# Kernel optimization log

Hardware: AMD Instinct MI355X
Metric: run time of the kernel (lower is better)

## Reference

```python
import jax, jax.numpy as jnp
import numpy as np

B, S, D = 2, 2048, 1024
H, KVH, HD = 16, 4, 64
ROPE_THETA = 10000.0


def rotate_half(x):
    h = x.shape[-1] // 2
    return jnp.concatenate([-x[..., h:], x[..., :h]], axis=-1)


def setup_inputs() -> dict:
    key = jax.random.key(0)
    k = jax.random.split(key, 6)
    x = jax.random.normal(k[0], (B, S, D), dtype=jnp.float32)
    # real RoPE tables: [S, HD//2]
    inv_freq = 1.0 / (ROPE_THETA ** (jnp.arange(0, HD, 2, dtype=jnp.float32) / HD))
    t = jnp.arange(S, dtype=jnp.float32)
    freqs = jnp.outer(t, inv_freq)  # [S, HD/2]
    cos = jnp.cos(freqs)
    sin = jnp.sin(freqs)
    # causal additive mask [1,1,S,S]
    neg = jnp.float32(-1e9)
    mask = jnp.where(jnp.tril(jnp.ones((S, S), dtype=bool)), 0.0, neg)[None, None]
    scale = 0.02
    wq = jax.random.normal(k[1], (D, H * HD), dtype=jnp.float32) * scale
    wk = jax.random.normal(k[2], (D, KVH * HD), dtype=jnp.float32) * scale
    wv = jax.random.normal(k[3], (D, KVH * HD), dtype=jnp.float32) * scale
    wo = jax.random.normal(k[4], (H * HD, D), dtype=jnp.float32) * scale
    return {"x": x, "cos": cos, "sin": sin, "mask": mask,
            "wq": wq, "wk": wk, "wv": wv, "wo": wo}


def reference(x, cos, sin, mask, wq, wk, wv, wo):
    b, s, d = x.shape
    hd = 2 * cos.shape[-1]
    h = wq.shape[1] // hd
    kvh = wk.shape[1] // hd
    n_rep = h // kvh

    q = (x @ wq).reshape(b, s, h, hd)
    k = (x @ wk).reshape(b, s, kvh, hd)
    v = (x @ wv).reshape(b, s, kvh, hd)

    # RoPE: cos/sin [S, hd/2] -> [1, s, 1, hd] via self-concat (rotate_half style)
    c = jnp.concatenate([cos[:s], cos[:s]], axis=-1)[None, :, None, :]
    sn = jnp.concatenate([sin[:s], sin[:s]], axis=-1)[None, :, None, :]
    q = q * c + rotate_half(q) * sn
    k = k * c + rotate_half(k) * sn

    new_k, new_v = k, v  # kv cache (pre-repeat)

    # GQA: repeat each kv head n_rep times contiguously (== expand+reshape)
    if n_rep > 1:
        k = jnp.repeat(k, n_rep, axis=2)
        v = jnp.repeat(v, n_rep, axis=2)

    scores = jnp.einsum('bqhd,bkhd->bhqk', q, k) / jnp.sqrt(jnp.float32(hd))
    scores = scores + mask
    attn = jax.nn.softmax(scores.astype(jnp.float32), axis=-1).astype(q.dtype)
    out = jnp.einsum('bhqk,bkhd->bqhd', attn, v).reshape(b, s, h * hd)
    out = out @ wo
    return (out, new_k, new_v)
```

## Files before the change

kernel.cpp:

```cpp
#include <hip/hip_runtime.h>
#include <hip/hip_bf16.h>

constexpr int B_ = 2, S_ = 2048, D_ = 1024, H_ = 16, KVH_ = 4, HD_ = 64;

typedef __attribute__((ext_vector_type(8))) short short8;
typedef __attribute__((ext_vector_type(4))) float f32x4;
typedef __attribute__((ext_vector_type(16))) float f32x16;

__device__ inline short f2b(float x) {
  unsigned u = __float_as_uint(x);
  return (short)((u + 0x7fffu + ((u >> 16) & 1u)) >> 16);
}
__device__ inline unsigned pkbf2(float lo, float hi) {
  __hip_bfloat162 h = __float22bfloat162_rn(float2{lo, hi});
  return *(unsigned*)&h;
}

__device__ inline void async16(void* lds, const void* g) {
  __builtin_amdgcn_global_load_lds(
      (const __attribute__((address_space(1))) unsigned int*)g,
      (__attribute__((address_space(3))) unsigned int*)lds, 16, 0, 0);
}

__global__ __launch_bounds__(256) void prep_kernel(
    const float* __restrict__ x, short* __restrict__ xb,
    const float* __restrict__ wq, const float* __restrict__ wk,
    const float* __restrict__ wv, const float* __restrict__ wo,
    short* __restrict__ wt, short* __restrict__ wot) {
  __shared__ short ts[64][66];
  const int tid = threadIdx.x;
  if (blockIdx.x < 4096) {
    const int idx = (blockIdx.x * 256 + tid) * 4;
    float4 v = *(const float4*)(x + idx);
    short4 o;
    o.x = f2b(v.x); o.y = f2b(v.y); o.z = f2b(v.z); o.w = f2b(v.w);
    *(short4*)(xb + idx) = o;
    return;
  }
  const int bid = blockIdx.x - 4096;
  const int z = bid >> 8, bi = (bid >> 4) & 15, bj = bid & 15;
  const float* W;
  short* dst;
  int N;
  if (z == 0)      { W = wq; dst = wt;                       N = 1024; }
  else if (z == 1) { W = wo; dst = wot;                      N = 1024; }
  else if (z == 2) { W = wk; dst = wt + (size_t)1024 * 1024; N = 256; }
  else             { W = wv; dst = wt + (size_t)1280 * 1024; N = 256; }
  if (bj * 64 >= N) return;
#pragma unroll
  for (int i = 0; i < 16; ++i) {
    int idx = tid + i * 256;
    int r = idx >> 6, c = idx & 63;
    ts[r][c] = f2b(W[(size_t)(bi * 64 + r) * N + bj * 64 + c]);
  }
  __syncthreads();
#pragma unroll
  for (int i = 0; i < 16; ++i) {
    int idx = tid + i * 256;
    int cc = idx >> 6, rr = idx & 63;
    dst[(size_t)(bj * 64 + cc) * 1024 + bi * 64 + rr] = ts[rr][cc];
  }
}

struct GemmLdsDb {
  short As[2][128][32];
  short Bs[2][128][32];
};

__device__ inline void gemm_core_db(GemmLdsDb& lds, const short* __restrict__ A,
                                    const short* __restrict__ Bt, int K,
                                    int row0, int col0, int tid,
                                    f32x4 (&acc)[4][4]) {
  const int w = tid >> 6, lane = tid & 63;
  const int grp = lane >> 4, li = lane & 15;
  const int wr = w & 1, wc = w >> 1;
  const int lr = lane >> 2, ls = (lane & 3) * 8;
#pragma unroll
  for (int mt = 0; mt < 4; ++mt)
#pragma unroll
    for (int nt = 0; nt < 4; ++nt) acc[mt][nt] = (f32x4){0.f, 0.f, 0.f, 0.f};

  auto issue = [&](int bi, int k0) {
#pragma unroll
    for (int i = 0; i < 2; ++i) {
      const int r = i * 64 + w * 16;
      async16(&lds.As[bi][r][0], A + (size_t)(row0 + r + lr) * K + k0 + ls);
      async16(&lds.Bs[bi][r][0], Bt + (size_t)(col0 + r + lr) * K + k0 + ls);
    }
  };

  issue(0, 0);
  const int nk = K >> 5;
  for (int kk = 0; kk < nk; ++kk) {
    const int cur = kk & 1;
    __syncthreads();
    if (kk + 1 < nk) issue(cur ^ 1, (kk + 1) << 5);

    short8 af[4], bf[4];
#pragma unroll
    for (int mt = 0; mt < 4; ++mt)
      af[mt] = *(const short8*)&lds.As[cur][wr * 64 + mt * 16 + li][grp * 8];
#pragma unroll
    for (int nt = 0; nt < 4; ++nt)
      bf[nt] = *(const short8*)&lds.Bs[cur][wc * 64 + nt * 16 + li][grp * 8];
#pragma unroll
    for (int mt = 0; mt < 4; ++mt)
#pragma unroll
      for (int nt = 0; nt < 4; ++nt)
        acc[mt][nt] = __builtin_amdgcn_mfma_f32_16x16x32_bf16(
            af[mt], bf[nt], acc[mt][nt], 0, 0, 0);
  }
}

#define QSCALE 0.1803368801111f

__global__ __launch_bounds__(256) void gemm_qkv(
    const short* __restrict__ A, const short* __restrict__ Bt,
    const float* __restrict__ cs, const float* __restrict__ sn,
    short* __restrict__ qb, float* __restrict__ koutp, short* __restrict__ kb,
    float* __restrict__ voutp, short* __restrict__ vbT) {
  __shared__ GemmLdsDb lds;
  const int tid = threadIdx.x;
  const int w = tid >> 6, lane = tid & 63;
  const int grp = lane >> 4, li = lane & 15;
  const int wr = w & 1, wc = w >> 1;
  const int row0 = blockIdx.y * 128, col0 = blockIdx.x * 128;
  f32x4 acc[4][4];
  gemm_core_db(lds, A, Bt, D_, row0, col0, tid, acc);

  if (col0 < 1024) {
#pragma unroll
    for (int mt = 0; mt < 4; ++mt)
#pragma unroll
      for (int r = 0; r < 4; ++r) {
        const int row = row0 + wr * 64 + mt * 16 + grp * 4 + r;
        const int spos = row & (S_ - 1);
#pragma unroll
        for (int nt = 0; nt < 2; ++nt) {
          const int col = col0 + wc * 64 + nt * 16 + li;
          const int d = col & 63;
          const float c = cs[spos * 32 + d];
          const float s = sn[spos * 32 + d];
          const float x0 = acc[mt][nt][r], x1 = acc[mt][nt + 2][r];
          qb[(size_t)row * 1024 + col] = f2b((x0 * c - x1 * s) * QSCALE);
          qb[(size_t)row * 1024 + col + 32] = f2b((x1 * c + x0 * s) * QSCALE);
        }
      }
  } else if (col0 < 1280) {
#pragma unroll
    for (int mt = 0; mt < 4; ++mt)
#pragma unroll
      for (int r = 0; r < 4; ++r) {
        const int row = row0 + wr * 64 + mt * 16 + grp * 4 + r;
        const int spos = row & (S_ - 1);
#pragma unroll
        for (int nt = 0; nt < 2; ++nt) {
          const int kcol = col0 + wc * 64 + nt * 16 + li - 1024;
          const int d = kcol & 63;
          const float c = cs[spos * 32 + d];
          const float s = sn[spos * 32 + d];
          const float x0 = acc[mt][nt][r], x1 = acc[mt][nt + 2][r];
          const float k0v = x0 * c - x1 * s;
          const float k1v = x1 * c + x0 * s;
          koutp[(size_t)row * 256 + kcol] = k0v;
          koutp[(size_t)row * 256 + kcol + 32] = k1v;
          kb[(size_t)row * 256 + kcol] = f2b(k0v);
          kb[(size_t)row * 256 + kcol + 32] = f2b(k1v);
        }
      }
  } else {
#pragma unroll
    for (int mt = 0; mt < 4; ++mt)
#pragma unroll
      for (int nt = 0; nt < 4; ++nt) {
        const int vcol = col0 + wc * 64 + nt * 16 + li - 1280;
        const int row_base = row0 + wr * 64 + mt * 16 + grp * 4;
        short4 pk;
        float vv[4];
#pragma unroll
        for (int r = 0; r < 4; ++r) vv[r] = acc[mt][nt][r];
        pk.x = f2b(vv[0]); pk.y = f2b(vv[1]);
        pk.z = f2b(vv[2]); pk.w = f2b(vv[3]);
#pragma unroll
        for (int r = 0; r < 4; ++r)
          voutp[(size_t)(row_base + r) * 256 + vcol] = vv[r];
        const int b = row_base >> 11, s0 = row_base & (S_ - 1);
        *(short4*)&vbT[((size_t)(b * 256 + vcol)) * S_ + s0] = pk;
      }
  }
}

__global__ __launch_bounds__(128) void fattn_kernel(
    const short* __restrict__ qb, const short* __restrict__ kb,
    const short* __restrict__ vbT, short* __restrict__ o) {
  __shared__ float scr[64 * 33 + 32];

  const int tid = threadIdx.x;
  const int par = tid >> 6, lane = tid & 63;
  const int n32 = lane & 31, kg = lane >> 5;

  const int qt = 63 - (blockIdx.x >> 5);
  const int bh = blockIdx.x & 31;
  const int b = bh >> 4, h = bh & 15, kh = h >> 2;
  const int qq = qt >> 1, st = qt & 1;
  const int nt = qq + 1;

  const short* qp =
      qb + ((size_t)(b * S_ + qt * 32 + n32)) * 1024 + h * 64 + kg * 8;
  short8 qa[4];
#pragma unroll
  for (int ks = 0; ks < 4; ++ks) qa[ks] = *(const short8*)(qp + ks * 16);

  const short* kl = kb + ((size_t)(b * S_) + n32) * 256 + kh * 64 + kg * 8;
  const short* vl0 = vbT + ((size_t)(b * 256 + kh * 64 + n32)) * S_ + kg * 8;
  const short* vl1 = vl0 + (size_t)32 * S_;

  f32x16 zero16;
#pragma unroll
  for (int i = 0; i < 16; ++i) zero16[i] = 0.f;
  f32x16 Oa0 = zero16, Oa1 = zero16;
  float lreg = 0.f;

  auto loadK = [&](int t, short8 (&kr)[8]) {
    const short* kt = kl + (size_t)t * (64 * 256);
#pragma unroll
    for (int i = 0; i < 4; ++i) {
      kr[i] = *(const short8*)(kt + i * 16);
      kr[i + 4] = *(const short8*)(kt + 32 * 256 + i * 16);
    }
  };

  auto body = [&](int t, const short8 (&kr)[8]) {
    const bool diag = (t == qq);
    const short* vt0 = vl0 + t * 64;
    const short* vt1 = vl1 + t * 64;
    short8 vr[8];
#pragma unroll
    for (int kc = 0; kc < 4; ++kc) {
      vr[kc] = *(const short8*)(vt0 + kc * 16);
      vr[kc + 4] = *(const short8*)(vt1 + kc * 16);
    }
    unsigned pk[4][4];
#pragma unroll
    for (int s = 0; s < 2; ++s) {
      if (s == 1 && diag && st == 0) continue;
      f32x16 sv = __builtin_amdgcn_mfma_f32_32x32x16_bf16(kr[s * 4 + 0], qa[0],
                                                          zero16, 0, 0, 0);
      sv = __builtin_amdgcn_mfma_f32_32x32x16_bf16(kr[s * 4 + 1], qa[1], sv, 0,
                                                   0, 0);
      sv = __builtin_amdgcn_mfma_f32_32x32x16_bf16(kr[s * 4 + 2], qa[2], sv, 0,
                                                   0, 0);
      sv = __builtin_amdgcn_mfma_f32_32x32x16_bf16(kr[s * 4 + 3], qa[3], sv, 0,
                                                   0, 0);
      const bool dm = diag && (s == st);
      float e[16];
#pragma unroll
      for (int rr = 0; rr < 16; ++rr) {
        float v = __builtin_amdgcn_exp2f(sv[rr]);
        if (dm) {
          const int key32 = (rr & 3) + 8 * (rr >> 2) + 4 * kg;
          if (key32 > n32) v = 0.f;
        }
        e[rr] = v;
      }
      pk[2 * s][0] = pkbf2(e[0], e[1]);
      pk[2 * s][1] = pkbf2(e[2], e[3]);
      pk[2 * s][2] = pkbf2(e[4], e[5]);
      pk[2 * s][3] = pkbf2(e[6], e[7]);
      pk[2 * s + 1][0] = pkbf2(e[8], e[9]);
      pk[2 * s + 1][1] = pkbf2(e[10], e[11]);
      pk[2 * s + 1][2] = pkbf2(e[12], e[13]);
      pk[2 * s + 1][3] = pkbf2(e[14], e[15]);
      lreg += (((e[0] + e[1]) + (e[2] + e[3])) +
               ((e[4] + e[5]) + (e[6] + e[7]))) +
              (((e[8] + e[9]) + (e[10] + e[11])) +
               ((e[12] + e[13]) + (e[14] + e[15])));
    }

    auto pv = [&](int kc) {
      auto r02 =
          __builtin_amdgcn_permlane32_swap(pk[kc][0], pk[kc][2], false, false);
      auto r13 =
          __builtin_amdgcn_permlane32_swap(pk[kc][1], pk[kc][3], false, false);
      union { unsigned u[4]; short8 s8; } f;
      f.u[0] = r02[0]; f.u[1] = r13[0]; f.u[2] = r02[1]; f.u[3] = r13[1];
      Oa0 = __builtin_amdgcn_mfma_f32_32x32x16_bf16(vr[kc], f.s8, Oa0, 0, 0, 0);
      Oa1 = __builtin_amdgcn_mfma_f32_32x32x16_bf16(vr[kc + 4], f.s8, Oa1, 0,
                                                    0, 0);
    };
    if (diag && st == 0) {
      pv(0); pv(1);
    } else {
      pv(0); pv(1); pv(2); pv(3);
    }
  };

  {
    short8 kA[8], kB[8];
    int t = par;
    if (t < nt) {
      loadK(t, kA);
      while (true) {
        {
          const int tp = (t + 2 < nt) ? t + 2 : t;
          loadK(tp, kB);
          body(t, kA);
          t += 2;
          if (t >= nt) break;
        }
        {
          const int tp = (t + 2 < nt) ? t + 2 : t;
          loadK(tp, kA);
          body(t, kB);
          t += 2;
          if (t >= nt) break;
        }
      }
    }
  }

  lreg += __shfl_xor(lreg, 32);

  float* lb = scr + 64 * 33;
  if (par == 1) {
#pragma unroll
    for (int rr = 0; rr < 16; ++rr) {
      const int d0 = (rr & 3) + 8 * (rr >> 2) + 4 * kg;
      scr[d0 * 33 + n32] = Oa0[rr];
      scr[(d0 + 32) * 33 + n32] = Oa1[rr];
    }
    if (kg == 0) lb[n32] = lreg;
  }
  __syncthreads();
  if (par == 0) {
    const float inv = __builtin_amdgcn_rcpf(lreg + lb[n32]);
#pragma unroll
    for (int rr = 0; rr < 16; ++rr) {
      const int d0 = (rr & 3) + 8 * (rr >> 2) + 4 * kg;
      scr[d0 * 33 + n32] = (Oa0[rr] + scr[d0 * 33 + n32]) * inv;
      scr[(d0 + 32) * 33 + n32] = (Oa1[rr] + scr[(d0 + 32) * 33 + n32]) * inv;
    }
  }
  __syncthreads();
  {
    const int q = tid >> 2, seg = (tid & 3) * 16;
    const size_t gb = ((size_t)(b * S_ + qt * 32 + q)) * 1024 + h * 64 + seg;
    short8 t0, t1;
#pragma unroll
    for (int k2 = 0; k2 < 8; ++k2) {
      t0[k2] = f2b(scr[(seg + k2) * 33 + q]);
      t1[k2] = f2b(scr[(seg + 8 + k2) * 33 + q]);
    }
    *(short8*)(o + gb) = t0;
    *(short8*)(o + gb + 8) = t1;
  }
}

__global__ __launch_bounds__(256) void gemm_bt_f32(
    const short* __restrict__ A, const short* __restrict__ Bt,
    float* __restrict__ C, int N, int K) {
  __shared__ GemmLdsDb lds;
  const int tid = threadIdx.x;
  const int w = tid >> 6, lane = tid & 63;
  const int grp = lane >> 4, li = lane & 15;
  const int wr = w & 1, wc = w >> 1;
  const int row0 = blockIdx.y * 128, col0 = blockIdx.x * 128;
  f32x4 acc[4][4];
  gemm_core_db(lds, A, Bt, K, row0, col0, tid, acc);
#pragma unroll
  for (int mt = 0; mt < 4; ++mt)
#pragma unroll
    for (int nt = 0; nt < 4; ++nt)
#pragma unroll
      for (int r = 0; r < 4; ++r)
        C[(size_t)(row0 + wr * 64 + mt * 16 + grp * 4 + r) * N + col0 +
          wc * 64 + nt * 16 + li] = acc[mt][nt][r];
}

extern "C" void kernel_launch(void* const* d_in, const int* in_sizes, int n_in,
                              void* d_out, int out_size, void* d_ws,
                              size_t ws_size, hipStream_t stream) {
  const float* x  = (const float*)d_in[0];
  const float* cs = (const float*)d_in[1];
  const float* sn = (const float*)d_in[2];
  const float* wq = (const float*)d_in[4];
  const float* wk = (const float*)d_in[5];
  const float* wv = (const float*)d_in[6];
  const float* wo = (const float*)d_in[7];

  float* outp  = (float*)d_out;
  float* koutp = outp + (size_t)B_ * S_ * H_ * HD_;
  float* voutp = koutp + (size_t)B_ * S_ * KVH_ * HD_;

  char* p = (char*)d_ws;
  short* xb   = (short*)p; p += (size_t)B_ * S_ * D_ * 2;
  short* qb   = (short*)p; p += (size_t)B_ * S_ * H_ * HD_ * 2;
  short* kb   = (short*)p; p += (size_t)B_ * S_ * KVH_ * HD_ * 2;
  short* vbT  = (short*)p; p += (size_t)B_ * S_ * KVH_ * HD_ * 2;
  short* abuf = (short*)p; p += (size_t)B_ * S_ * H_ * HD_ * 2;
  short* wt   = (short*)p; p += (size_t)1536 * D_ * 2;
  short* wot  = (short*)p; p += (size_t)D_ * H_ * HD_ * 2;

  const int M = B_ * S_;

  prep_kernel<<<4096 + 1024, 256, 0, stream>>>(x, xb, wq, wk, wv, wo, wt,
                                               wot);

  gemm_qkv<<<dim3(1536 / 128, M / 128), 256, 0, stream>>>(
      xb, wt, cs, sn, qb, koutp, kb, voutp, vbT);

  fattn_kernel<<<64 * 32, 128, 0, stream>>>(qb, kb, vbT, abuf);

  gemm_bt_f32<<<dim3(1024 / 128, M / 128), 256, 0, stream>>>(abuf, wot, outp,
                                                             1024, 1024);
}
```

Before: 211.2 us.

## Store K and V in MFMA fragment-contiguous tiled layout for coalesced attention loads

The projection kernel now writes bf16 K and transposed V into a per-(batch,kv-head) tiled layout where each lane's 16-byte MFMA operand sits contiguously, so the attention kernel loads fragments with lane-linear, fully coalesced addresses instead of strided row accesses. The K prefetch for tile t+2 is moved inside the body after the V loads and made conditional, removing the redundant reload of the current tile at the end of the loop. The cost is scattered 2-byte stores in the prep kernel's epilogue, which may hurt write coalescing there.

```diff
diff --git a/kernel.cpp b/kernel.cpp
--- a/kernel.cpp
+++ b/kernel.cpp
@@ -152,11 +152,12 @@
 #pragma unroll
       for (int r = 0; r < 4; ++r) {
         const int row = row0 + wr * 64 + mt * 16 + grp * 4 + r;
-        const int spos = row & (S_ - 1);
+        const int bq = row >> 11, spos = row & (S_ - 1);
+        const int sb = spos >> 5, k32 = spos & 31;
 #pragma unroll
         for (int nt = 0; nt < 2; ++nt) {
           const int kcol = col0 + wc * 64 + nt * 16 + li - 1024;
-          const int d = kcol & 63;
+          const int khk = kcol >> 6, d = kcol & 63;
           const float c = cs[spos * 32 + d];
           const float s = sn[spos * 32 + d];
           const float x0 = acc[mt][nt][r], x1 = acc[mt][nt + 2][r];
@@ -164,8 +165,11 @@
           const float k1v = x1 * c + x0 * s;
           koutp[(size_t)row * 256 + kcol] = k0v;
           koutp[(size_t)row * 256 + kcol + 32] = k1v;
-          kb[(size_t)row * 256 + kcol] = f2b(k0v);
-          kb[(size_t)row * 256 + kcol + 32] = f2b(k1v);
+          short* kbase =
+              kb + (((size_t)(bq * 4 + khk) * 64 + sb) * 2048) + k32 * 8;
+          const int d2 = d + 32;
+          kbase[((d >> 4) * 2 + ((d >> 3) & 1)) * 256 + (d & 7)] = f2b(k0v);
+          kbase[((d2 >> 4) * 2 + ((d2 >> 3) & 1)) * 256 + (d2 & 7)] = f2b(k1v);
         }
       }
   } else {
@@ -184,8 +188,13 @@
 #pragma unroll
         for (int r = 0; r < 4; ++r)
           voutp[(size_t)(row_base + r) * 256 + vcol] = vv[r];
-        const int b = row_base >> 11, s0 = row_base & (S_ - 1);
-        *(short4*)&vbT[((size_t)(b * 256 + vcol)) * S_ + s0] = pk;
+        const int bq = row_base >> 11, s0 = row_base & (S_ - 1);
+        const int t = s0 >> 6, k64 = s0 & 63;
+        const int kc = k64 >> 4, kg8 = (k64 >> 3) & 1, k8 = k64 & 7;
+        const int khv = vcol >> 6, d = vcol & 63;
+        short* vb = vbT + (((size_t)(bq * 4 + khv) * 32 + t) * 4096) +
+                    (d >> 5) * 2048 + kc * 512 + kg8 * 256 + (d & 31) * 8 + k8;
+        *(short4*)vb = pk;
       }
   }
 }
@@ -211,9 +220,8 @@
 #pragma unroll
   for (int ks = 0; ks < 4; ++ks) qa[ks] = *(const short8*)(qp + ks * 16);
 
-  const short* kl = kb + ((size_t)(b * S_) + n32) * 256 + kh * 64 + kg * 8;
-  const short* vl0 = vbT + ((size_t)(b * 256 + kh * 64 + n32)) * S_ + kg * 8;
-  const short* vl1 = vl0 + (size_t)32 * S_;
+  const short* kF = kb + ((size_t)(b * 4 + kh) << 17) + lane * 8;
+  const short* vF = vbT + ((size_t)(b * 4 + kh) << 17) + lane * 8;
 
   f32x16 zero16;
 #pragma unroll
@@ -222,24 +230,25 @@
   float lreg = 0.f;
 
   auto loadK = [&](int t, short8 (&kr)[8]) {
-    const short* kt = kl + (size_t)t * (64 * 256);
-#pragma unroll
-    for (int i = 0; i < 4; ++i) {
-      kr[i] = *(const short8*)(kt + i * 16);
-      kr[i + 4] = *(const short8*)(kt + 32 * 256 + i * 16);
-    }
+    const short* kt = kF + (size_t)t * 4096;
+#pragma unroll
+    for (int s = 0; s < 2; ++s)
+#pragma unroll
+      for (int ks = 0; ks < 4; ++ks)
+        kr[s * 4 + ks] = *(const short8*)(kt + s * 2048 + ks * 512);
   };
 
-  auto body = [&](int t, const short8 (&kr)[8]) {
+  auto body = [&](int t, const short8 (&kr)[8], short8 (&knx)[8]) {
     const bool diag = (t == qq);
-    const short* vt0 = vl0 + t * 64;
-    const short* vt1 = vl1 + t * 64;
+    const short* vt = vF + (size_t)t * 4096;
     short8 vr[8];
 #pragma unroll
     for (int kc = 0; kc < 4; ++kc) {
-      vr[kc] = *(const short8*)(vt0 + kc * 16);
-      vr[kc + 4] = *(const short8*)(vt1 + kc * 16);
-    }
+      vr[kc] = *(const short8*)(vt + kc * 512);
+      vr[kc + 4] = *(const short8*)(vt + 2048 + kc * 512);
+    }
+    if (t + 2 < nt) loadK(t + 2, knx);
+
     unsigned pk[4][4];
 #pragma unroll
     for (int s = 0; s < 2; ++s) {
@@ -300,21 +309,13 @@
     int t = par;
     if (t < nt) {
       loadK(t, kA);
-      while (true) {
-        {
-          const int tp = (t + 2 < nt) ? t + 2 : t;
-          loadK(tp, kB);
-          body(t, kA);
-          t += 2;
-          if (t >= nt) break;
-        }
-        {
-          const int tp = (t + 2 < nt) ? t + 2 : t;
-          loadK(tp, kA);
-          body(t, kB);
-          t += 2;
-          if (t >= nt) break;
-        }
+      for (;;) {
+        body(t, kA, kB);
+        t += 2;
+        if (t >= nt) break;
+        body(t, kB, kA);
+        t += 2;
+        if (t >= nt) break;
       }
     }
   }
```

Measured after the change: 171.7 us, median of 2. -18.7%, faster.
